# Kernel tuning notes

Hardware: AMD Instinct MI355X
Metric: run time of the kernel (lower is better)

Reference implementation:

```python
import jax, jax.numpy as jnp
import numpy as np

TOP_K = 16
MEMORY_SIZE = 256
FEAT_DIM = 512
PROMPT_SHAPE = (64, 2048)
BATCH = 512
EPS = 1e-8  # torch cosine_similarity norm clamp


def setup_inputs() -> dict:
    key = jax.random.key(0)
    k1, k2, k3 = jax.random.split(key, 3)
    features = jax.random.normal(k1, (BATCH, FEAT_DIM), dtype=jnp.float32)
    keys = jax.random.normal(k2, (MEMORY_SIZE, FEAT_DIM), dtype=jnp.float32)
    memory = jax.random.normal(k3, (MEMORY_SIZE,) + PROMPT_SHAPE, dtype=jnp.float32)
    return {"features": features, "keys": keys, "memory": memory}


def reference(features, keys, memory):
    # Cosine similarity of each feature vs every memory key: (B, M)
    f_n = features / jnp.maximum(jnp.linalg.norm(features, axis=-1, keepdims=True), EPS)
    k_n = keys / jnp.maximum(jnp.linalg.norm(keys, axis=-1, keepdims=True), EPS)
    sim = f_n @ k_n.T  # (B, M)

    # top-k per sample, clamp negatives to 0, renormalize
    top_sim, top_ids = jax.lax.top_k(sim, TOP_K)  # (B, K)
    top_sim = jnp.maximum(top_sim, 0.0)
    w = top_sim / jnp.sum(top_sim, axis=-1, keepdims=True)  # (B, K)

    # Weighted gather-sum over memory bank, expressed as sparse-weight GEMM:
    # scatter per-sample weights into a (B, M) matrix, then contract with memory.
    B = w.shape[0]
    W = jnp.zeros((B, MEMORY_SIZE), dtype=w.dtype)
    W = W.at[jnp.arange(B)[:, None], top_ids].add(w)
    ctx = jnp.einsum('bm,mpq->bpq', W, memory)  # (B, 64, 2048)
    return ctx
```

## Files before the change

kernel.cpp:

```cpp
#include <hip/hip_runtime.h>

#define FEAT   512
#define MEMN   256
#define BATCH  512
#define PROMPT 131072
#define TOPK   16
#define EPSF   1e-8f

#define CCOLS  32
#define NCH    32
#define NGRP   128
#define BT     128
#define NTILE  4

__global__ __launch_bounds__(256) void knorm_kernel(
    const float* __restrict__ keys, float* __restrict__ kn)
{
    __shared__ float red[4];
    const int m = blockIdx.x;
    const int tid = threadIdx.x;
    float2 v = *reinterpret_cast<const float2*>(keys + m * FEAT + tid * 2);
    float p = v.x * v.x + v.y * v.y;
    for (int off = 32; off; off >>= 1) p += __shfl_down(p, off);
    if ((tid & 63) == 0) red[tid >> 6] = p;
    __syncthreads();
    float s = red[0] + red[1] + red[2] + red[3];
    float nrm = sqrtf(s); if (nrm < EPSF) nrm = EPSF;
    const float inv = 1.0f / nrm;
    float2 o; o.x = v.x * inv; o.y = v.y * inv;
    *reinterpret_cast<float2*>(kn + m * FEAT + tid * 2) = o;
}

__global__ __launch_bounds__(256) void topk_kernel(
    const float* __restrict__ features,
    const float* __restrict__ kn,
    int* __restrict__ out_ids,
    float* __restrict__ out_w)
{
    __shared__ float f_lds[FEAT];
    __shared__ float sim_lds[MEMN];
    __shared__ float red[4];

    const int b = blockIdx.x;
    const int tid = threadIdx.x;

    float2 fv = *reinterpret_cast<const float2*>(features + b * FEAT + tid * 2);
    *reinterpret_cast<float2*>(f_lds + tid * 2) = fv;
    float p = fv.x * fv.x + fv.y * fv.y;
    for (int off = 32; off; off >>= 1) p += __shfl_down(p, off);
    if ((tid & 63) == 0) red[tid >> 6] = p;
    __syncthreads();
    const float f2 = red[0] + red[1] + red[2] + red[3];
    float fn = sqrtf(f2); if (fn < EPSF) fn = EPSF;
    const float invf = 1.0f / fn;

    const int wave = tid >> 6, lane = tid & 63;
    const int jc = lane & 15, msub = lane >> 4;
    for (int pss = 0; pss < 16; ++pss) {
        const int m = pss * 16 + wave * 4 + msub;
        const float* krow = kn + m * FEAT;
        float dot = 0.f;
#pragma unroll
        for (int s = 0; s < 8; ++s) {
            float4 kv = *reinterpret_cast<const float4*>(krow + s * 64 + jc * 4);
            float4 fw = *reinterpret_cast<const float4*>(f_lds + s * 64 + jc * 4);
            dot += kv.x * fw.x + kv.y * fw.y + kv.z * fw.z + kv.w * fw.w;
        }
        dot += __shfl_xor(dot, 1); dot += __shfl_xor(dot, 2);
        dot += __shfl_xor(dot, 4); dot += __shfl_xor(dot, 8);
        if (jc == 0) sim_lds[m] = dot * invf;
    }
    __syncthreads();

    if (tid < 64) {
        const int lane_ = tid;
        float v0 = sim_lds[lane_];
        float v1 = sim_lds[lane_ + 64];
        float v2 = sim_lds[lane_ + 128];
        float v3 = sim_lds[lane_ + 192];
        int myid = 0;

        for (int r = 0; r < TOPK; ++r) {
            float bv = v0; int bi = lane_;
            if (v1 > bv) { bv = v1; bi = lane_ + 64;  }
            if (v2 > bv) { bv = v2; bi = lane_ + 128; }
            if (v3 > bv) { bv = v3; bi = lane_ + 192; }
            for (int off = 32; off > 0; off >>= 1) {
                const float ov = __shfl_down(bv, off);
                const int   oi = __shfl_down(bi, off);
                if (ov > bv || (ov == bv && oi < bi)) { bv = ov; bi = oi; }
            }
            bi = __shfl(bi, 0);
            if (lane_ == r) myid = bi;
            if ((bi & 63) == lane_) {
                const int slot = bi >> 6;
                if      (slot == 0) v0 = -1e30f;
                else if (slot == 1) v1 = -1e30f;
                else if (slot == 2) v2 = -1e30f;
                else                v3 = -1e30f;
            }
        }

        if (lane_ < TOPK) {
            float val = sim_lds[myid];
            if (val < 0.f) val = 0.f;
            float s = val;
            for (int off = 1; off < TOPK; off <<= 1)
                s += __shfl_xor(s, off);
            out_ids[b * TOPK + lane_] = myid;
            out_w[b * TOPK + lane_]   = val / s;
        }
    }
}

__global__ __launch_bounds__(256, 2) void ctx_kernel(
    const float* __restrict__ mem,
    const int* __restrict__ ids,
    const float* __restrict__ wgt,
    float* __restrict__ out)
{
    __shared__ float slab0[MEMN * CCOLS];
    __shared__ float slab1[MEMN * CCOLS];

    const int bid  = blockIdx.x;
    const int xcd  = bid & 7;
    const int idx  = bid >> 3;
    const int tile = idx >> 4;
    const int g    = xcd * 16 + (idx & 15);
    const int b_base = tile * BT;
    const int col0   = g * (NCH * CCOLS);

    const int tid  = threadIdx.x;
    const int wave = tid >> 6, lane = tid & 63;
    const int bg   = lane >> 3;
    const int cg   = lane & 7;

    const int bA = b_base + wave * 8 + bg;

    int   off[4 * TOPK];
    float w[4 * TOPK];
#pragma unroll
    for (int q = 0; q < 4; ++q) {
        const int b = bA + q * 32;
#pragma unroll
        for (int r = 0; r < 4; ++r) {
            int4   iv = *reinterpret_cast<const int4*>(ids + b * TOPK + r * 4);
            float4 wv = *reinterpret_cast<const float4*>(wgt + b * TOPK + r * 4);
            off[q*16 + r*4 + 0] = iv.x * (CCOLS*4) + cg * 16;
            off[q*16 + r*4 + 1] = iv.y * (CCOLS*4) + cg * 16;
            off[q*16 + r*4 + 2] = iv.z * (CCOLS*4) + cg * 16;
            off[q*16 + r*4 + 3] = iv.w * (CCOLS*4) + cg * 16;
            w[q*16 + r*4 + 0] = wv.x; w[q*16 + r*4 + 1] = wv.y;
            w[q*16 + r*4 + 2] = wv.z; w[q*16 + r*4 + 3] = wv.w;
        }
    }

    auto stage = [&](float* buf, int cb) {
#pragma unroll
        for (int i = 0; i < 8; ++i) {
            const int r = wave * 64 + i * 8 + bg;
            const float* gp = mem + (size_t)r * PROMPT + cb + cg * 4;
            float* lp = buf + (wave * 64 + i * 8) * CCOLS + lane * 4;
            __builtin_amdgcn_global_load_lds(
                (const __attribute__((address_space(1))) unsigned int*)gp,
                (__attribute__((address_space(3))) unsigned int*)lp,
                16, 0, 0);
        }
    };

    auto compute = [&](const float* buf, int cb) {
        const char* slb = reinterpret_cast<const char*>(buf);
#pragma unroll
        for (int q = 0; q < 4; ++q) {
            float4 acc;
            acc.x = acc.y = acc.z = acc.w = 0.f;
#pragma unroll
            for (int k = 0; k < TOPK; ++k) {
                const float4 v = *reinterpret_cast<const float4*>(slb + off[q*16 + k]);
                const float ww = w[q*16 + k];
                acc.x += ww * v.x; acc.y += ww * v.y;
                acc.z += ww * v.z; acc.w += ww * v.w;
            }
            const int b = bA + q * 32;
            *reinterpret_cast<float4*>(out + (size_t)b * PROMPT + cb + cg * 4) = acc;
        }
    };

    stage(slab0, col0);
    asm volatile("s_waitcnt vmcnt(0)" ::: "memory");
    __builtin_amdgcn_s_barrier();
    asm volatile("" ::: "memory");

    for (int c = 0; c < NCH; c += 2) {
        stage(slab1, col0 + (c + 1) * CCOLS);
        asm volatile("" ::: "memory");
        compute(slab0, col0 + c * CCOLS);
        asm volatile("s_waitcnt vmcnt(4)" ::: "memory");
        __builtin_amdgcn_s_barrier();
        asm volatile("" ::: "memory");

        if (c + 2 < NCH) stage(slab0, col0 + (c + 2) * CCOLS);
        asm volatile("" ::: "memory");
        compute(slab1, col0 + (c + 1) * CCOLS);
        asm volatile("s_waitcnt vmcnt(4)" ::: "memory");
        __builtin_amdgcn_s_barrier();
        asm volatile("" ::: "memory");
    }
}

extern "C" void kernel_launch(void* const* d_in, const int* in_sizes, int n_in,
                              void* d_out, int out_size, void* d_ws, size_t ws_size,
                              hipStream_t stream) {
    const float* features = (const float*)d_in[0];
    const float* keys     = (const float*)d_in[1];
    const float* mem      = (const float*)d_in[2];
    float* out = (float*)d_out;

    char* ws = (char*)d_ws;
    int*   ids = (int*)ws;
    float* wgt = (float*)(ws + 32768);
    float* kn  = (float*)(ws + 65536);

    knorm_kernel<<<MEMN, 256, 0, stream>>>(keys, kn);
    topk_kernel<<<BATCH, 256, 0, stream>>>(features, kn, ids, wgt);
    ctx_kernel<<<NTILE * NGRP, 256, 0, stream>>>(mem, ids, wgt, out);
}
```

Baseline: 469.6 us.

## Split similarity into batched-tile GEMM kernel and separate top-k select kernel

Replaces the key-normalize and per-sample top-k kernels with a tiled similarity kernel and a lightweight selection kernel. Each similarity block computes 8 samples against 32 keys, so every key row read from global memory is reused across 8 features. The key norm is computed inline, which removes the separate normalize pass. The feature norm is dropped because it does not change top-k order or the renormalized weights, except when a feature norm falls below eps. The cost is an extra global round-trip of the similarity matrix and one additional launch, while ctx_kernel, which dominates runtime, is unchanged.

```diff
diff --git a/kernel.cpp b/kernel.cpp
--- a/kernel.cpp
+++ b/kernel.cpp
@@ -7,109 +7,122 @@
 #define TOPK   16
 #define EPSF   1e-8f
 
+#define SB 8
+#define SK 32
+
 #define CCOLS  32
 #define NCH    32
 #define NGRP   128
 #define BT     128
 #define NTILE  4
 
-__global__ __launch_bounds__(256) void knorm_kernel(
-    const float* __restrict__ keys, float* __restrict__ kn)
+__global__ __launch_bounds__(256) void sim_kernel(
+    const float* __restrict__ features,
+    const float* __restrict__ keys,
+    float* __restrict__ sim)
 {
-    __shared__ float red[4];
-    const int m = blockIdx.x;
+    __shared__ float f_lds[SB * FEAT];
+
+    const int bg = blockIdx.x >> 3;
+    const int kg = blockIdx.x & 7;
+    const int b0 = bg * SB;
+    const int k0 = kg * SK;
     const int tid = threadIdx.x;
-    float2 v = *reinterpret_cast<const float2*>(keys + m * FEAT + tid * 2);
-    float p = v.x * v.x + v.y * v.y;
-    for (int off = 32; off; off >>= 1) p += __shfl_down(p, off);
-    if ((tid & 63) == 0) red[tid >> 6] = p;
+
+    {
+        const int r = tid >> 5, c = tid & 31;
+#pragma unroll
+        for (int q = 0; q < 4; ++q) {
+            float4 v = *reinterpret_cast<const float4*>(
+                features + (size_t)(b0 + r) * FEAT + (c + q * 32) * 4);
+            *reinterpret_cast<float4*>(f_lds + r * FEAT + (c + q * 32) * 4) = v;
+        }
+    }
     __syncthreads();
-    float s = red[0] + red[1] + red[2] + red[3];
-    float nrm = sqrtf(s); if (nrm < EPSF) nrm = EPSF;
-    const float inv = 1.0f / nrm;
-    float2 o; o.x = v.x * inv; o.y = v.y * inv;
-    *reinterpret_cast<float2*>(kn + m * FEAT + tid * 2) = o;
-}
-
-__global__ __launch_bounds__(256) void topk_kernel(
-    const float* __restrict__ features,
-    const float* __restrict__ kn,
+
+    const int wave = tid >> 6, lane = tid & 63;
+    const int jc = lane & 15, msub = lane >> 4;
+
+#pragma unroll
+    for (int p = 0; p < 2; ++p) {
+        const int mloc = p * 16 + wave * 4 + msub;
+        const float* krow = keys + (size_t)(k0 + mloc) * FEAT;
+        float dot[SB];
+        float kk = 0.f;
+#pragma unroll
+        for (int b = 0; b < SB; ++b) dot[b] = 0.f;
+#pragma unroll
+        for (int s = 0; s < 8; ++s) {
+            float4 kv = *reinterpret_cast<const float4*>(krow + s * 64 + jc * 4);
+            kk += kv.x * kv.x + kv.y * kv.y + kv.z * kv.z + kv.w * kv.w;
+#pragma unroll
+            for (int b = 0; b < SB; ++b) {
+                float4 fw = *reinterpret_cast<const float4*>(
+                    f_lds + b * FEAT + s * 64 + jc * 4);
+                dot[b] += kv.x * fw.x + kv.y * fw.y + kv.z * fw.z + kv.w * fw.w;
+            }
+        }
+#pragma unroll
+        for (int b = 0; b < SB; ++b) {
+            dot[b] += __shfl_xor(dot[b], 1); dot[b] += __shfl_xor(dot[b], 2);
+            dot[b] += __shfl_xor(dot[b], 4); dot[b] += __shfl_xor(dot[b], 8);
+        }
+        kk += __shfl_xor(kk, 1); kk += __shfl_xor(kk, 2);
+        kk += __shfl_xor(kk, 4); kk += __shfl_xor(kk, 8);
+
+        if (jc == 0) {
+            float nrm = sqrtf(kk); if (nrm < EPSF) nrm = EPSF;
+            const float inv = 1.0f / nrm;
+#pragma unroll
+            for (int b = 0; b < SB; ++b)
+                sim[(size_t)(b0 + b) * MEMN + k0 + mloc] = dot[b] * inv;
+        }
+    }
+}
+
+__global__ __launch_bounds__(64) void select_kernel(
+    const float* __restrict__ sim,
     int* __restrict__ out_ids,
     float* __restrict__ out_w)
 {
-    __shared__ float f_lds[FEAT];
-    __shared__ float sim_lds[MEMN];
-    __shared__ float red[4];
-
     const int b = blockIdx.x;
-    const int tid = threadIdx.x;
-
-    float2 fv = *reinterpret_cast<const float2*>(features + b * FEAT + tid * 2);
-    *reinterpret_cast<float2*>(f_lds + tid * 2) = fv;
-    float p = fv.x * fv.x + fv.y * fv.y;
-    for (int off = 32; off; off >>= 1) p += __shfl_down(p, off);
-    if ((tid & 63) == 0) red[tid >> 6] = p;
-    __syncthreads();
-    const float f2 = red[0] + red[1] + red[2] + red[3];
-    float fn = sqrtf(f2); if (fn < EPSF) fn = EPSF;
-    const float invf = 1.0f / fn;
-
-    const int wave = tid >> 6, lane = tid & 63;
-    const int jc = lane & 15, msub = lane >> 4;
-    for (int pss = 0; pss < 16; ++pss) {
-        const int m = pss * 16 + wave * 4 + msub;
-        const float* krow = kn + m * FEAT;
-        float dot = 0.f;
-#pragma unroll
-        for (int s = 0; s < 8; ++s) {
-            float4 kv = *reinterpret_cast<const float4*>(krow + s * 64 + jc * 4);
-            float4 fw = *reinterpret_cast<const float4*>(f_lds + s * 64 + jc * 4);
-            dot += kv.x * fw.x + kv.y * fw.y + kv.z * fw.z + kv.w * fw.w;
-        }
-        dot += __shfl_xor(dot, 1); dot += __shfl_xor(dot, 2);
-        dot += __shfl_xor(dot, 4); dot += __shfl_xor(dot, 8);
-        if (jc == 0) sim_lds[m] = dot * invf;
-    }
-    __syncthreads();
-
-    if (tid < 64) {
-        const int lane_ = tid;
-        float v0 = sim_lds[lane_];
-        float v1 = sim_lds[lane_ + 64];
-        float v2 = sim_lds[lane_ + 128];
-        float v3 = sim_lds[lane_ + 192];
-        int myid = 0;
-
-        for (int r = 0; r < TOPK; ++r) {
-            float bv = v0; int bi = lane_;
-            if (v1 > bv) { bv = v1; bi = lane_ + 64;  }
-            if (v2 > bv) { bv = v2; bi = lane_ + 128; }
-            if (v3 > bv) { bv = v3; bi = lane_ + 192; }
-            for (int off = 32; off > 0; off >>= 1) {
-                const float ov = __shfl_down(bv, off);
-                const int   oi = __shfl_down(bi, off);
-                if (ov > bv || (ov == bv && oi < bi)) { bv = ov; bi = oi; }
-            }
-            bi = __shfl(bi, 0);
-            if (lane_ == r) myid = bi;
-            if ((bi & 63) == lane_) {
-                const int slot = bi >> 6;
-                if      (slot == 0) v0 = -1e30f;
-                else if (slot == 1) v1 = -1e30f;
-                else if (slot == 2) v2 = -1e30f;
-                else                v3 = -1e30f;
-            }
-        }
-
-        if (lane_ < TOPK) {
-            float val = sim_lds[myid];
-            if (val < 0.f) val = 0.f;
-            float s = val;
-            for (int off = 1; off < TOPK; off <<= 1)
-                s += __shfl_xor(s, off);
-            out_ids[b * TOPK + lane_] = myid;
-            out_w[b * TOPK + lane_]   = val / s;
-        }
+    const int lane_ = threadIdx.x;
+
+    float v0 = sim[(size_t)b * MEMN + lane_];
+    float v1 = sim[(size_t)b * MEMN + lane_ + 64];
+    float v2 = sim[(size_t)b * MEMN + lane_ + 128];
+    float v3 = sim[(size_t)b * MEMN + lane_ + 192];
+    int myid = 0;
+
+    for (int r = 0; r < TOPK; ++r) {
+        float bv = v0; int bi = lane_;
+        if (v1 > bv) { bv = v1; bi = lane_ + 64;  }
+        if (v2 > bv) { bv = v2; bi = lane_ + 128; }
+        if (v3 > bv) { bv = v3; bi = lane_ + 192; }
+        for (int off = 32; off > 0; off >>= 1) {
+            const float ov = __shfl_down(bv, off);
+            const int   oi = __shfl_down(bi, off);
+            if (ov > bv || (ov == bv && oi < bi)) { bv = ov; bi = oi; }
+        }
+        bi = __shfl(bi, 0);
+        if (lane_ == r) myid = bi;
+        if ((bi & 63) == lane_) {
+            const int slot = bi >> 6;
+            if      (slot == 0) v0 = -1e30f;
+            else if (slot == 1) v1 = -1e30f;
+            else if (slot == 2) v2 = -1e30f;
+            else                v3 = -1e30f;
+        }
+    }
+
+    if (lane_ < TOPK) {
+        float val = sim[(size_t)b * MEMN + myid];
+        if (val < 0.f) val = 0.f;
+        float s = val;
+        for (int off = 1; off < TOPK; off <<= 1)
+            s += __shfl_xor(s, off);
+        out_ids[b * TOPK + lane_] = myid;
+        out_w[b * TOPK + lane_]   = val / s;
     }
 }
 
@@ -160,7 +173,7 @@
         for (int i = 0; i < 8; ++i) {
             const int r = wave * 64 + i * 8 + bg;
             const float* gp = mem + (size_t)r * PROMPT + cb + cg * 4;
-            float* lp = buf + (wave * 64 + i * 8) * CCOLS + lane * 4;
+            float* lp = buf + (size_t)(wave * 64 + i * 8) * CCOLS + lane * 4;
             __builtin_amdgcn_global_load_lds(
                 (const __attribute__((address_space(1))) unsigned int*)gp,
                 (__attribute__((address_space(3))) unsigned int*)lp,
@@ -219,9 +232,9 @@
     char* ws = (char*)d_ws;
     int*   ids = (int*)ws;
     float* wgt = (float*)(ws + 32768);
-    float* kn  = (float*)(ws + 65536);
-
-    knorm_kernel<<<MEMN, 256, 0, stream>>>(keys, kn);
-    topk_kernel<<<BATCH, 256, 0, stream>>>(features, kn, ids, wgt);
+    float* sim = (float*)(ws + 65536);
+
+    sim_kernel<<<(BATCH / SB) * (MEMN / SK), 256, 0, stream>>>(features, keys, sim);
+    select_kernel<<<BATCH, 64, 0, stream>>>(sim, ids, wgt);
     ctx_kernel<<<NTILE * NGRP, 256, 0, stream>>>(mem, ids, wgt, out);
 }
```

Result: faster. 451.8 us (-3.8%).
